# Optimization experiments

Measured on AMD Instinct MI355X. Metric: run time of the kernel, lower is better.

The kernel has to match this reference:

```python
import jax, jax.numpy as jnp
import numpy as np
from jax import lax

N = 2048
NUM_CLASSES = 21  # background + 20 classes


def xy_to_cxcy(xy):
    return jnp.concatenate([(xy[:, 2:] + xy[:, :2]) / 2.0, xy[:, 2:] - xy[:, :2]], axis=-1)


def cxcy_to_xy(c):
    return jnp.concatenate([c[:, :2] - c[:, 2:] / 2.0, c[:, :2] + c[:, 2:] / 2.0], axis=-1)


def gcxgcy_to_cxcy(g, priors_cxcy):
    # offsets already pre-scaled (/10, /20) by the caller, matching the torch forward
    return jnp.concatenate([g[:, :2] * priors_cxcy[:, 2:] + priors_cxcy[:, :2],
                            jnp.exp(g[:, 2:]) * priors_cxcy[:, 2:]], axis=-1)


def pairwise_iou(a, b):
    # a: [N,4], b: [M,4] corner format -> [N,M]
    lt = jnp.maximum(a[:, None, :2], b[None, :, :2])
    rb = jnp.minimum(a[:, None, 2:], b[None, :, 2:])
    wh = jnp.clip(rb - lt, 0.0)
    inter = wh[..., 0] * wh[..., 1]
    area_a = (a[:, 2] - a[:, 0]) * (a[:, 3] - a[:, 1])
    area_b = (b[:, 2] - b[:, 0]) * (b[:, 3] - b[:, 1])
    return inter / (area_a[:, None] + area_b[None, :] - inter)


def _detect(rois_xy, predicted_locs, predicted_scores, min_score, max_overlap, top_k):
    n = rois_xy.shape[0]
    rois_cxcy = xy_to_cxcy(rois_xy)
    locs = predicted_locs.reshape(n, -1, 4)                      # [N, C, 4]
    probs = jax.nn.softmax(predicted_scores, axis=1)             # [N, C]
    best = jnp.argmax(probs, axis=1)                             # locs for argmax class
    g = jnp.take_along_axis(locs, best[:, None, None], axis=1)[:, 0, :]
    g = jnp.concatenate([g[:, :2] / 10.0, g[:, 2:] / 20.0], axis=-1)
    decoded = cxcy_to_xy(gcxgcy_to_cxcy(g, rois_cxcy))           # [N, 4]

    def nms_class(cls_scores):
        valid = cls_scores > min_score
        s = jnp.where(valid, cls_scores, -jnp.inf)
        order = jnp.argsort(-s)                                  # desc; invalid last
        s_sorted = s[order]
        b_sorted = decoded[order]
        ov = lax.stop_gradient(pairwise_iou(b_sorted, b_sorted))  # [N, N]
        sup0 = ~valid[order]                                     # invalid start suppressed

        def body(i, sup):
            new = jnp.logical_or(sup, ov[i] > max_overlap)
            new = new.at[i].set(False)                           # never self-suppress
            return jnp.where(sup[i], sup, new)                   # skip already-suppressed

        sup = lax.fori_loop(0, n, body, sup0)
        return b_sorted, jnp.where(~sup, s_sorted, -jnp.inf)

    # vmap the greedy NMS over the 20 foreground classes
    boxes_c, scores_c = jax.vmap(nms_class)(probs[:, 1:].T)      # [20,N,4], [20,N]
    labels_c = jnp.broadcast_to(jnp.arange(1, NUM_CLASSES)[:, None], scores_c.shape)

    fs = scores_c.reshape(-1)
    fb = boxes_c.reshape(-1, 4)
    fl = labels_c.reshape(-1)
    topv, topi = lax.top_k(fs, top_k)
    ok = jnp.isfinite(topv)
    out_boxes = jnp.where(ok[:, None], fb[topi],
                          jnp.array([0.0, 0.0, 1.0, 1.0], dtype=fb.dtype))
    out_labels = jnp.where(ok, fl[topi], 0)
    out_scores = jnp.where(ok, topv, 0.0)
    return out_boxes, out_labels, out_scores


def setup_inputs() -> dict:
    key = jax.random.key(0)
    k1, k2, k3, k4 = jax.random.split(key, 4)
    cxcy = jax.random.uniform(k1, (N, 2), minval=0.1, maxval=0.9)
    wh = jax.random.uniform(k2, (N, 2), minval=0.05, maxval=0.3)
    rois_xy = jnp.concatenate([cxcy - wh / 2.0, cxcy + wh / 2.0], axis=-1)
    predicted_locs = jax.random.normal(k3, (N, NUM_CLASSES * 4), dtype=jnp.float32) * 0.5
    predicted_scores = jax.random.normal(k4, (N, NUM_CLASSES), dtype=jnp.float32) * 2.0
    return {"rois_xy": rois_xy,
            "predicted_locs": predicted_locs,
            "predicted_scores": predicted_scores,
            "min_score": jnp.float32(0.01),
            "max_overlap": jnp.float32(0.45),
            "top_k": 100}


def reference(rois_xy, predicted_locs, predicted_scores, min_score, max_overlap, top_k):
    return _detect(rois_xy, predicted_locs, predicted_scores, min_score, max_overlap, top_k)
```

## Files before the change

kernel.cpp:

```cpp
#include <hip/hip_runtime.h>
#include <cstdint>

#define NROI 2048
#define NCLS 21
#define NFG  20
#define CPAD 128
#define CTOT (NFG * CPAD)
#define NTHR 1024
#define SBLK 256
#define RSEL 384
#define SCAP 512
#define CSEL 512
#define DROWS 64
#define INVH 0xFF800000u

typedef unsigned long long u64;
typedef unsigned int u32;

__device__ __forceinline__ u32 desc_key(float s) {
  u32 u = __float_as_uint(s);
  u32 asc = (u & 0x80000000u) ? ~u : (u | 0x80000000u);
  return ~asc;
}
__device__ __forceinline__ float key_to_float(u32 desc) {
  u32 asc = ~desc;
  u32 u = (asc & 0x80000000u) ? (asc ^ 0x80000000u) : ~asc;
  return __uint_as_float(u);
}
__device__ __forceinline__ u64 shflx_u64(u64 v, int m) {
  u32 lo = (u32)v, hi = (u32)(v >> 32);
  lo = (u32)__shfl_xor((int)lo, m);
  hi = (u32)__shfl_xor((int)hi, m);
  return ((u64)hi << 32) | (u64)lo;
}
__device__ __forceinline__ void cmpex64(u64& mine, u64 other, int i, int j, int k) {
  bool amIlow = ((i & j) == 0);
  bool dir = ((i & k) == 0);
  bool otherLess = other < mine;
  if (otherLess != (amIlow != dir)) mine = other;
}

__device__ __forceinline__ void bucket_select(const int* h, int need, int lane,
                                              int* outB, int* outC) {
  int base = lane << 2;
  int c0 = h[base], c1 = h[base + 1], c2 = h[base + 2], c3 = h[base + 3];
  int s = c0 + c1 + c2 + c3;
  int pre = s;
  #pragma unroll
  for (int off = 1; off < 64; off <<= 1) {
    int v = __shfl_up(pre, off);
    if (lane >= off) pre += v;
  }
  u64 ball = __ballot(pre >= need);
  int ln = __ffsll((long long)ball) - 1;
  int exc = __shfl(pre, ln) - __shfl(s, ln);
  int b0 = __shfl(c0, ln), b1 = __shfl(c1, ln), b2 = __shfl(c2, ln);
  int bkt, cb;
  if (exc + b0 >= need)                { bkt = (ln << 2) + 0; cb = exc; }
  else if (exc + b0 + b1 >= need)      { bkt = (ln << 2) + 1; cb = exc + b0; }
  else if (exc + b0 + b1 + b2 >= need) { bkt = (ln << 2) + 2; cb = exc + b0 + b1; }
  else                                 { bkt = (ln << 2) + 3; cb = exc + b0 + b1 + b2; }
  if (lane == 0) { *outB = bkt; *outC = cb; }
}

__global__ __launch_bounds__(64)
void k_decode(const float* __restrict__ rois,
              const float* __restrict__ locs,
              const float* __restrict__ scores,
              float* __restrict__ probsT,
              float4* __restrict__ decoded,
              u32* __restrict__ done) {
  __shared__ float srow[DROWS][NCLS + 2];
  const int tid = threadIdx.x;
  const int rbase = blockIdx.x * DROWS;
  if (rbase == 0 && tid == 0) *done = 0u;

  const float* src = scores + (size_t)rbase * NCLS;
  for (int t = tid; t < DROWS * NCLS; t += 64)
    srow[t / NCLS][t % NCLS] = src[t];
  __syncthreads();

  const int r = rbase + tid;
  float s[NCLS];
  #pragma unroll
  for (int c = 0; c < NCLS; ++c) s[c] = srow[tid][c];
  float m = s[0];
  #pragma unroll
  for (int c = 0; c < NCLS; ++c) m = fmaxf(m, s[c]);
  float sum = 0.0f;
  #pragma unroll
  for (int c = 0; c < NCLS; ++c) { s[c] = expf(s[c] - m); sum += s[c]; }

  float pb = s[0] / sum; int best = 0;
  #pragma unroll
  for (int c = 1; c < NCLS; ++c) {
    float p = s[c] / sum;
    probsT[(c - 1) * NROI + r] = p;
    if (p > pb) { pb = p; best = c; }
  }

  float4 roi = ((const float4*)rois)[r];
  float pcx = __fmul_rn(__fadd_rn(roi.x, roi.z), 0.5f);
  float pcy = __fmul_rn(__fadd_rn(roi.y, roi.w), 0.5f);
  float pw  = __fsub_rn(roi.z, roi.x);
  float ph  = __fsub_rn(roi.w, roi.y);

  float4 gl = ((const float4*)locs)[r * NCLS + best];
  float g0 = gl.x / 10.0f;
  float g1 = gl.y / 10.0f;
  float g2 = gl.z / 20.0f;
  float g3 = gl.w / 20.0f;

  float cx = __fadd_rn(__fmul_rn(g0, pw), pcx);
  float cy = __fadd_rn(__fmul_rn(g1, ph), pcy);
  float w  = __fmul_rn(expf(g2), pw);
  float h  = __fmul_rn(expf(g3), ph);
  float hw = __fmul_rn(w, 0.5f);
  float hh = __fmul_rn(h, 0.5f);
  decoded[r] = make_float4(__fsub_rn(cx, hw), __fsub_rn(cy, hh),
                           __fadd_rn(cx, hw), __fadd_rn(cy, hh));
}

__global__ __launch_bounds__(NTHR)
void k_nms(const float* __restrict__ probsT,
           const float4* __restrict__ decoded,
           const float* __restrict__ min_score_p,
           const float* __restrict__ max_overlap_p,
           u64* __restrict__ cand,
           float4* __restrict__ cbox,
           u32* __restrict__ done,
           float* __restrict__ out,
           const int* __restrict__ top_k_p) {
  __shared__ u32 LDSW[7168];
  __shared__ u64 remInitW[4];
  __shared__ int hist1[256], hist2[256];
  __shared__ int cntLds, scLds, cSelSh, selB1, selC1, selB2, selD2, mSh, cCnt;
  __shared__ u32 lastSh;

  u64* mbAu    = (u64*)(LDSW + 0);
  u64* mbBu    = (u64*)(LDSW + 1024);
  u64* skeyW64 = (u64*)(LDSW + 2048);
  u64* maskW   = (u64*)(LDSW + 3072);
  float* bx0   = (float*)(LDSW + 5120);
  float* by0   = (float*)(LDSW + 5376);
  float* bx1   = (float*)(LDSW + 5632);
  float* by1   = (float*)(LDSW + 5888);
  float* areaA = (float*)(LDSW + 6144);
  float* sx0   = (float*)(LDSW + 6400);
  float* sy0   = (float*)(LDSW + 6528);
  float* sx1   = (float*)(LDSW + 6656);
  float* sy1   = (float*)(LDSW + 6784);
  float* sarea = (float*)(LDSW + 6912);
  u32* survKeyH = LDSW + 7040;

  const int cls = blockIdx.x;
  const int tid = threadIdx.x;
  const int lane = tid & 63;
  const int wid = tid >> 6;
  const float msc = *min_score_p;
  const float ovr = *max_overlap_p;
  const int K = *top_k_p;
  const int Kcap = (K < CPAD) ? K : CPAD;

  if (tid == 0) { cntLds = 0; scLds = 0; }
  __syncthreads();

  float p0v = probsT[cls * NROI + tid];
  float p1v = probsT[cls * NROI + tid + 1024];
  bool v0 = p0v > msc, v1 = p1v > msc;
  u64 kq0 = ((u64)desc_key(v0 ? p0v : -__builtin_inff()) << 32) | (u32)tid;
  u64 kq1 = ((u64)desc_key(v1 ? p1v : -__builtin_inff()) << 32) | (u32)(tid + 1024);
  {
    u64 ba = __ballot(v0), bb = __ballot(v1);
    if (lane == 0) atomicAdd(&cntLds, __popcll(ba) + __popcll(bb));
  }
  __syncthreads();
  const int nv = cntLds;

  int sc = 0;
  int processed = 0;
  u64 minKey = 0ULL;

  while (sc < Kcap && processed < nv) {
    int rem = nv - processed;
    int need = (rem < RSEL) ? rem : RSEL;

    if (tid < 256) { hist1[tid] = 0; hist2[tid] = 0; }
    if (tid == 0) cSelSh = 0;
    __syncthreads();
    bool val0 = (kq0 > minKey) && ((u32)(kq0 >> 32) < INVH);
    bool val1 = (kq1 > minKey) && ((u32)(kq1 >> 32) < INVH);
    if (val0) atomicAdd(&hist1[(int)((kq0 >> 56) & 255)], 1);
    if (val1) atomicAdd(&hist1[(int)((kq1 >> 56) & 255)], 1);
    __syncthreads();
    if (wid == 0) bucket_select(hist1, need, lane, &selB1, &selC1);
    __syncthreads();
    const int B1 = selB1, C1 = selC1;
    if (val0 && (int)((kq0 >> 56) & 255) == B1)
      atomicAdd(&hist2[(int)((kq0 >> 48) & 255)], 1);
    if (val1 && (int)((kq1 >> 56) & 255) == B1)
      atomicAdd(&hist2[(int)((kq1 >> 48) & 255)], 1);
    __syncthreads();
    if (wid == 0) bucket_select(hist2, need - C1, lane, &selB2, &selD2);
    __syncthreads();
    const int pred16 = (selB1 << 8) | selB2;

    bool s0 = val0 && (int)((kq0 >> 48) & 0xFFFF) <= pred16;
    bool s1 = val1 && (int)((kq1 >> 48) & 0xFFFF) <= pred16;
    {
      u64 b0 = __ballot(s0), b1 = __ballot(s1);
      int cnt = __popcll(b0) + __popcll(b1);
      int basePos = 0;
      if (lane == 0) basePos = cnt ? atomicAdd(&cSelSh, cnt) : 0;
      basePos = __shfl(basePos, 0);
      u64 lm = (lane == 63) ? ~0ULL >> 1 : ((1ULL << lane) - 1ULL);
      lm = (1ULL << lane) - 1ULL;
      int p0 = basePos + __popcll(b0 & lm);
      int p1 = basePos + __popcll(b0) + __popcll(b1 & lm);
      if (s0 && p0 < SCAP) mbAu[p0] = kq0;
      if (s1 && p1 < SCAP) mbAu[p1] = kq1;
    }
    __syncthreads();
    int Csel = cSelSh; if (Csel > SCAP) Csel = SCAP;
    if (tid < SCAP && tid >= Csel) mbAu[tid] = ~0ULL;
    __syncthreads();

    u64 key = (tid < SCAP) ? mbAu[tid] : ~0ULL;
    int parity = 0;
    auto ldsp = [&](int k, int j) {
      u64* buf = parity ? mbBu : mbAu; parity ^= 1;
      if (tid < SCAP) buf[tid] = key;
      __syncthreads();
      if (tid < SCAP) { u64 o = buf[tid ^ j]; cmpex64(key, o, tid, j, k); }
    };
    auto shfp = [&](int k, int j) {
      if (tid < SCAP) { u64 o = shflx_u64(key, j); cmpex64(key, o, tid, j, k); }
    };
    for (int k = 2; k <= 64; k <<= 1)
      for (int j = k >> 1; j >= 1; j >>= 1) shfp(k, j);
    ldsp(128, 64);
    for (int j = 32; j >= 1; j >>= 1) shfp(128, j);
    ldsp(256, 128); ldsp(256, 64);
    for (int j = 32; j >= 1; j >>= 1) shfp(256, j);
    ldsp(512, 256); ldsp(512, 128); ldsp(512, 64);
    for (int j = 32; j >= 1; j >>= 1) shfp(512, j);
    if (tid < SCAP) skeyW64[tid] = key;
    __syncthreads();

    for (int base = 0; base < Csel && sc < Kcap; base += SBLK) {
      int RL = Csel - base; if (RL > SBLK) RL = SBLK;
      if (tid < SBLK) {
        int p = base + tid; if (p > Csel - 1) p = Csel - 1;
        u64 kq = skeyW64[p];
        float4 b = decoded[(u32)kq];
        bx0[tid] = b.x; by0[tid] = b.y; bx1[tid] = b.z; by1[tid] = b.w;
        areaA[tid] = __fmul_rn(__fsub_rn(b.z, b.x), __fsub_rn(b.w, b.y));
      }
      if (tid < 4) remInitW[tid] = 0ULL;
      __syncthreads();

      if (sc > 0 && tid < SBLK) {
        float jx0 = bx0[tid], jy0 = by0[tid], jx1 = bx1[tid], jy1 = by1[tid];
        float ab = areaA[tid];
        bool kill = false;
        for (int u = 0; u < sc; ++u) {
          float ix0 = sx0[u], iy0 = sy0[u], ix1 = sx1[u], iy1 = sy1[u];
          float ia = sarea[u];
          float lx = fmaxf(ix0, jx0), ly = fmaxf(iy0, jy0);
          float rx = fminf(ix1, jx1), ry = fminf(iy1, jy1);
          float w_ = fmaxf(__fsub_rn(rx, lx), 0.0f);
          float h_ = fmaxf(__fsub_rn(ry, ly), 0.0f);
          float inter = __fmul_rn(w_, h_);
          float iou = __fdiv_rn(inter, __fsub_rn(__fadd_rn(ia, ab), inter));
          kill = kill || (iou > ovr);
        }
        u64 bal = __ballot(kill);
        if (lane == 0) remInitW[wid] = bal;
      }

      {
        int nw = (RL + 63) >> 6;
        for (int r2 = wid; r2 < RL; r2 += 16) {
          float ix0 = bx0[r2], iy0 = by0[r2], ix1 = bx1[r2], iy1 = by1[r2];
          float ia = areaA[r2];
          for (int ct = (r2 >> 6); ct < nw; ++ct) {
            int j = (ct << 6) + lane;
            float jx0 = bx0[j], jy0 = by0[j], jx1 = bx1[j], jy1 = by1[j];
            float ab = areaA[j];
            float lx = fmaxf(ix0, jx0), ly = fmaxf(iy0, jy0);
            float rx = fminf(ix1, jx1), ry = fminf(iy1, jy1);
            float w_ = fmaxf(__fsub_rn(rx, lx), 0.0f);
            float h_ = fmaxf(__fsub_rn(ry, ly), 0.0f);
            float inter = __fmul_rn(w_, h_);
            float iou = __fdiv_rn(inter, __fsub_rn(__fadd_rn(ia, ab), inter));
            bool bit = iou > ovr;
            if (ct == (r2 >> 6)) bit = bit && (j > r2);
            u64 bal = __ballot(bit);
            if (lane == 0) maskW[(r2 << 2) + ct] = bal;
          }
        }
      }
      __syncthreads();

      if (wid == 0) {
        int t0 = RL;
        u64 rw0 = (t0 <= 0) ? ~0ULL : ((t0 >= 64) ? 0ULL : (~0ULL << t0));
        int t1 = t0 - 64;
        u64 rw1 = (t1 <= 0) ? ~0ULL : ((t1 >= 64) ? 0ULL : (~0ULL << t1));
        int t2 = t0 - 128;
        u64 rw2 = (t2 <= 0) ? ~0ULL : ((t2 >= 64) ? 0ULL : (~0ULL << t2));
        int t3 = t0 - 192;
        u64 rw3 = (t3 <= 0) ? ~0ULL : ((t3 >= 64) ? 0ULL : (~0ULL << t3));
        rw0 |= remInitW[0]; rw1 |= remInitW[1];
        rw2 |= remInitW[2]; rw3 |= remInitW[3];
        int scW = sc;
        bool full = scW >= Kcap;
#define SWEEPG(G, RWG)                                                        \
        if (!full) {                                                          \
          u64 pend = ~(RWG);                                                  \
          while (pend && !full) {                                             \
            int b = __ffsll((long long)pend) - 1;                             \
            int row = ((G) << 6) + b;                                         \
            u64 m0 = maskW[(row << 2) + 0], m1 = maskW[(row << 2) + 1];       \
            u64 m2 = maskW[(row << 2) + 2], m3 = maskW[(row << 2) + 3];       \
            rw0 |= m0; rw1 |= m1; rw2 |= m2; rw3 |= m3;                       \
            pend &= ~(1ULL << b);                                             \
            pend &= ~((G) == 0 ? m0 : (G) == 1 ? m1 : (G) == 2 ? m2 : m3);    \
            u32 hsv = (u32)(skeyW64[base + row] >> 32);                       \
            if (lane == 0) {                                                  \
              survKeyH[scW] = hsv;                                            \
              sx0[scW] = bx0[row]; sy0[scW] = by0[row];                       \
              sx1[scW] = bx1[row]; sy1[scW] = by1[row];                       \
              sarea[scW] = areaA[row];                                        \
            }                                                                 \
            ++scW;                                                            \
            full = scW >= Kcap;                                               \
          }                                                                   \
        }
        SWEEPG(0, rw0) SWEEPG(1, rw1) SWEEPG(2, rw2) SWEEPG(3, rw3)
#undef SWEEPG
        if (lane == 0) scLds = scW;
      }
      __syncthreads();
      sc = scLds;
    }

    minKey = skeyW64[Csel - 1];
    processed += Csel;
    __syncthreads();
  }

  if (tid < CPAD) {
    int o = cls * CPAD + tid;
    if (tid < sc) {
      cand[o] = ((u64)survKeyH[tid] << 32) | (u32)o;
      cbox[o] = make_float4(sx0[tid], sy0[tid], sx1[tid], sy1[tid]);
    } else {
      cand[o] = ~0ULL;
    }
  }

  __threadfence();
  __syncthreads();
  if (tid == 0) lastSh = atomicAdd(done, 1u);
  __syncthreads();
  if (lastSh != NFG - 1) return;
  __threadfence();

  u64* kk = (u64*)LDSW;
  u64* ck = (u64*)(LDSW + 5120);
  if (tid == 0) cCnt = 0;
  if (tid < 256) { hist1[tid] = 0; hist2[tid] = 0; }
  __syncthreads();
  for (int t = tid; t < CTOT; t += NTHR) {
    u64 v = cand[t];
    kk[t] = v;
    if (v != ~0ULL) atomicAdd(&hist1[(int)(v >> 56)], 1);
  }
  __syncthreads();
  if (wid == 0) {
    int b4 = lane << 2;
    int s = hist1[b4] + hist1[b4 + 1] + hist1[b4 + 2] + hist1[b4 + 3];
    #pragma unroll
    for (int off = 32; off; off >>= 1) s += __shfl_xor(s, off);
    if (lane == 0) mSh = s;
  }
  __syncthreads();
  const int M = mSh;
  const int Kneed = (K < M) ? K : M;

  if (Kneed > 0) {
    if (wid == 0) bucket_select(hist1, Kneed, lane, &selB1, &selC1);
    __syncthreads();
    const int B1 = selB1, C1 = selC1;
    for (int t = tid; t < CTOT; t += NTHR) {
      u64 v = kk[t];
      if (v != ~0ULL && (int)(v >> 56) == B1)
        atomicAdd(&hist2[(int)((v >> 48) & 255)], 1);
    }
    __syncthreads();
    if (wid == 0) bucket_select(hist2, Kneed - C1, lane, &selB2, &selD2);
    __syncthreads();
    const int B2 = selB2;
    for (int t = tid; t < CTOT; t += NTHR) {
      u64 v = kk[t];
      if (v == ~0ULL) continue;
      int b1 = (int)(v >> 56);
      int b2 = (int)((v >> 48) & 255);
      if (b1 < B1 || (b1 == B1 && b2 <= B2)) {
        int pos = atomicAdd(&cCnt, 1);
        if (pos < CSEL) ck[pos] = v;
      }
    }
    __syncthreads();
    const int C = cCnt;
    if (C <= CSEL) {
      if (tid < C) {
        u64 my = ck[tid];
        int rank = 0;
        for (int u = 0; u < C; ++u) rank += (ck[u] < my) ? 1 : 0;
        if (rank < K) {
          u32 flat = (u32)(my & 0xFFFFFFFFu);
          float score = key_to_float((u32)(my >> 32));
          int c2 = (int)(flat >> 7);
          float4 b = cbox[flat];
          out[rank * 4 + 0] = b.x;
          out[rank * 4 + 1] = b.y;
          out[rank * 4 + 2] = b.z;
          out[rank * 4 + 3] = b.w;
          out[K * 4 + rank] = (float)(c2 + 1);
          out[K * 5 + rank] = score;
        }
      }
    } else {
      for (int t = tid; t < CTOT; t += NTHR) {
        u64 kap = kk[t];
        if (kap == ~0ULL) continue;
        int rank = 0;
        #pragma unroll
        for (int cc2 = 0; cc2 < NFG; ++cc2) {
          const u64* a = kk + cc2 * CPAD;
          int lb = 0;
          #pragma unroll
          for (int s2 = CPAD >> 1; s2; s2 >>= 1) {
            int pq = lb + s2;
            if (a[pq - 1] < kap) lb = pq;
          }
          rank += lb;
        }
        if (rank < K) {
          u32 flat = (u32)(kap & 0xFFFFFFFFu);
          float score = key_to_float((u32)(kap >> 32));
          int c2 = (int)(flat >> 7);
          float4 b = cbox[flat];
          out[rank * 4 + 0] = b.x;
          out[rank * 4 + 1] = b.y;
          out[rank * 4 + 2] = b.z;
          out[rank * 4 + 3] = b.w;
          out[K * 4 + rank] = (float)(c2 + 1);
          out[K * 5 + rank] = score;
        }
      }
    }
  }
  __syncthreads();
  for (int r = tid; r < K; r += NTHR) {
    if (r >= M) {
      out[r * 4 + 0] = 0.0f; out[r * 4 + 1] = 0.0f;
      out[r * 4 + 2] = 1.0f; out[r * 4 + 3] = 1.0f;
      out[K * 4 + r] = 0.0f;
      out[K * 5 + r] = 0.0f;
    }
  }
}

extern "C" void kernel_launch(void* const* d_in, const int* in_sizes, int n_in,
                              void* d_out, int out_size, void* d_ws, size_t ws_size,
                              hipStream_t stream) {
  const float* rois        = (const float*)d_in[0];
  const float* locs        = (const float*)d_in[1];
  const float* scores      = (const float*)d_in[2];
  const float* min_score   = (const float*)d_in[3];
  const float* max_overlap = (const float*)d_in[4];
  const int*   top_k       = (const int*)d_in[5];

  char* ws = (char*)d_ws;
  u64*    cand    = (u64*)ws;
  float4* cbox    = (float4*)(ws + 20480);
  float*  probsT  = (float*)(ws + 20480 + 40960);
  float4* decoded = (float4*)(ws + 20480 + 40960 + 163840);
  u32*    done    = (u32*)(ws + 20480 + 40960 + 163840 + 32768);

  k_decode<<<NROI / DROWS, 64, 0, stream>>>(rois, locs, scores, probsT, decoded, done);
  k_nms<<<NFG, NTHR, 0, stream>>>(probsT, decoded, min_score, max_overlap,
                                  cand, cbox, done, (float*)d_out, top_k);
}
```

Baseline: 69.03 us.

## Pipeline NMS mask sweep with prefetched rows and deferred parallel survivor copy

Rewrites the serial single-wave NMS sweep so it walks rows in order with software-prefetched mask words instead of find-first-set loops. Survivor box and key copies are deferred to a parallel pass by all threads, using a new survRows index buffer. Rows already suppressed by earlier survivors now skip building their IoU mask. RSEL rises from 384 to 480, and an extra barrier is added so the mask build can read remInitW. The trade-off is that the sweep visits every row rather than only pending ones, and there is one more barrier, plus slightly more LDS.

```diff
diff --git a/kernel.cpp b/kernel.cpp
--- a/kernel.cpp
+++ b/kernel.cpp
@@ -8,7 +8,7 @@
 #define CTOT (NFG * CPAD)
 #define NTHR 1024
 #define SBLK 256
-#define RSEL 384
+#define RSEL 480
 #define SCAP 512
 #define CSEL 512
 #define DROWS 64
@@ -131,7 +131,7 @@
            u32* __restrict__ done,
            float* __restrict__ out,
            const int* __restrict__ top_k_p) {
-  __shared__ u32 LDSW[7168];
+  __shared__ u32 LDSW[7296];
   __shared__ u64 remInitW[4];
   __shared__ int hist1[256], hist2[256];
   __shared__ int cntLds, scLds, cSelSh, selB1, selC1, selB2, selD2, mSh, cCnt;
@@ -152,6 +152,7 @@
   float* sy1   = (float*)(LDSW + 6784);
   float* sarea = (float*)(LDSW + 6912);
   u32* survKeyH = LDSW + 7040;
+  u32* survRows = LDSW + 7168;
 
   const int cls = blockIdx.x;
   const int tid = threadIdx.x;
@@ -213,8 +214,7 @@
       int basePos = 0;
       if (lane == 0) basePos = cnt ? atomicAdd(&cSelSh, cnt) : 0;
       basePos = __shfl(basePos, 0);
-      u64 lm = (lane == 63) ? ~0ULL >> 1 : ((1ULL << lane) - 1ULL);
-      lm = (1ULL << lane) - 1ULL;
+      u64 lm = (1ULL << lane) - 1ULL;
       int p0 = basePos + __popcll(b0 & lm);
       int p1 = basePos + __popcll(b0) + __popcll(b1 & lm);
       if (s0 && p0 < SCAP) mbAu[p0] = kq0;
@@ -277,10 +277,12 @@
         u64 bal = __ballot(kill);
         if (lane == 0) remInitW[wid] = bal;
       }
+      __syncthreads();
 
       {
         int nw = (RL + 63) >> 6;
         for (int r2 = wid; r2 < RL; r2 += 16) {
+          if ((remInitW[r2 >> 6] >> (r2 & 63)) & 1ULL) continue;
           float ix0 = bx0[r2], iy0 = by0[r2], ix1 = bx1[r2], iy1 = by1[r2];
           float ia = areaA[r2];
           for (int ct = (r2 >> 6); ct < nw; ++ct) {
@@ -315,34 +317,54 @@
         rw2 |= remInitW[2]; rw3 |= remInitW[3];
         int scW = sc;
         bool full = scW >= Kcap;
-#define SWEEPG(G, RWG)                                                        \
-        if (!full) {                                                          \
-          u64 pend = ~(RWG);                                                  \
-          while (pend && !full) {                                             \
-            int b = __ffsll((long long)pend) - 1;                             \
-            int row = ((G) << 6) + b;                                         \
-            u64 m0 = maskW[(row << 2) + 0], m1 = maskW[(row << 2) + 1];       \
-            u64 m2 = maskW[(row << 2) + 2], m3 = maskW[(row << 2) + 3];       \
-            rw0 |= m0; rw1 |= m1; rw2 |= m2; rw3 |= m3;                       \
-            pend &= ~(1ULL << b);                                             \
-            pend &= ~((G) == 0 ? m0 : (G) == 1 ? m1 : (G) == 2 ? m2 : m3);    \
-            u32 hsv = (u32)(skeyW64[base + row] >> 32);                       \
-            if (lane == 0) {                                                  \
-              survKeyH[scW] = hsv;                                            \
-              sx0[scW] = bx0[row]; sy0[scW] = by0[row];                       \
-              sx1[scW] = bx1[row]; sy1[scW] = by1[row];                       \
-              sarea[scW] = areaA[row];                                        \
-            }                                                                 \
-            ++scW;                                                            \
-            full = scW >= Kcap;                                               \
-          }                                                                   \
+        u64 a00,a01,a02,a03,a10,a11,a12,a13,a20,a21,a22,a23,a30,a31,a32,a33;
+        u64 b00,b01,b02,b03,b10,b11,b12,b13,b20,b21,b22,b23,b30,b31,b32,b33;
+#define LD4(V0,V1,V2,V3,R) { int rr_ = (R); \
+        V0 = maskW[(rr_<<2)+0]; V1 = maskW[(rr_<<2)+1]; \
+        V2 = maskW[(rr_<<2)+2]; V3 = maskW[(rr_<<2)+3]; }
+#define PRX(RWG, BIT, M0,M1,M2,M3, ROW) \
+        if (!full && !(((RWG) >> (BIT)) & 1ULL)) { \
+          rw0 |= (M0); rw1 |= (M1); rw2 |= (M2); rw3 |= (M3); \
+          if (lane == 0) survRows[scW] = (u32)(base + (ROW)); \
+          ++scW; full = (scW >= Kcap); \
+        }
+#define SWEEPG(G, RWG) \
+        if (!full && (((G) << 6) < RL)) { \
+          const int rb = (G) << 6; \
+          LD4(a00,a01,a02,a03, rb+0) LD4(a10,a11,a12,a13, rb+1) \
+          LD4(a20,a21,a22,a23, rb+2) LD4(a30,a31,a32,a33, rb+3) \
+          for (int bb = 0; bb < 64 && !full; bb += 4) { \
+            LD4(b00,b01,b02,b03, rb+bb+4) LD4(b10,b11,b12,b13, rb+bb+5) \
+            LD4(b20,b21,b22,b23, rb+bb+6) LD4(b30,b31,b32,b33, rb+bb+7) \
+            PRX(RWG, bb+0, a00,a01,a02,a03, rb+bb+0) \
+            PRX(RWG, bb+1, a10,a11,a12,a13, rb+bb+1) \
+            PRX(RWG, bb+2, a20,a21,a22,a23, rb+bb+2) \
+            PRX(RWG, bb+3, a30,a31,a32,a33, rb+bb+3) \
+            a00=b00;a01=b01;a02=b02;a03=b03; a10=b10;a11=b11;a12=b12;a13=b13; \
+            a20=b20;a21=b21;a22=b22;a23=b23; a30=b30;a31=b31;a32=b32;a33=b33; \
+          } \
         }
         SWEEPG(0, rw0) SWEEPG(1, rw1) SWEEPG(2, rw2) SWEEPG(3, rw3)
 #undef SWEEPG
+#undef PRX
+#undef LD4
         if (lane == 0) scLds = scW;
       }
       __syncthreads();
-      sc = scLds;
+
+      {
+        int scNew = scLds;
+        if (tid >= sc && tid < scNew) {
+          int wrow = (int)survRows[tid];
+          int rr = wrow - base;
+          sx0[tid] = bx0[rr]; sy0[tid] = by0[rr];
+          sx1[tid] = bx1[rr]; sy1[tid] = by1[rr];
+          sarea[tid] = areaA[rr];
+          survKeyH[tid] = (u32)(skeyW64[wrow] >> 32);
+        }
+        __syncthreads();
+        sc = scNew;
+      }
     }
 
     minKey = skeyW64[Csel - 1];
```

After: 58.08 us (median of 2 runs). -15.9%, faster.
